# Kernel optimization log

Measured on AMD Instinct MI355X. Metric: run time of the kernel, lower is better.

## Reference

```python
import jax, jax.numpy as jnp
import numpy as np

EPS = 1e-5


def _shift1d(x, s, axis):
    """out[..., y, ...] = linear interp of x at position y + s along `axis`,
    zero-padded outside (== grid_sample bilinear, padding_mode='zeros',
    align_corners=True, for a pure axis-aligned shift of s pixels)."""
    n = x.shape[axis]
    f = jnp.floor(s)
    frac = (s - f).astype(x.dtype)  # scalar in [0,1)
    fi = f.astype(jnp.int32)

    def gather(off):
        idx = jnp.arange(n) + fi + off
        mask = (idx >= 0) & (idx < n)
        v = jnp.take(x, jnp.clip(idx, 0, n - 1), axis=axis)
        mshape = [1] * x.ndim
        mshape[axis] = n
        return v * mask.reshape(mshape).astype(x.dtype)

    return (1 - frac) * gather(0) + frac * gather(1)


def _axial_dw(x, w_h, w_w, r):
    """ContinuousAxialDW: x + depthwise learnable-dilation conv along H and W.
    w_h, w_w: (C, k) per-channel taps."""
    r = jnp.maximum(r, 1.0)
    c = x.shape[1]
    kh = w_h.shape[1]
    kw = w_w.shape[1]
    acc_h = jnp.zeros_like(x)
    for i, off in enumerate(range(-(kh // 2), kh // 2 + 1)):
        acc_h = acc_h + _shift1d(x, off * r, 2) * w_h[:, i].reshape(1, c, 1, 1)
    acc_w = jnp.zeros_like(x)
    for i, off in enumerate(range(-(kw // 2), kw // 2 + 1)):
        acc_w = acc_w + _shift1d(x, off * r, 3) * w_w[:, i].reshape(1, c, 1, 1)
    return x + acc_h + acc_w


def _bn(x, g, b, m, v):
    sh = (1, -1, 1, 1)
    scale = g.reshape(sh) * jax.lax.rsqrt(v.reshape(sh) + EPS)
    return (x - m.reshape(sh)) * scale + b.reshape(sh)


def _prelu(x, a):
    return jnp.where(x >= 0, x, a.reshape(1, -1, 1, 1) * x)


def _pw(w, x):  # 1x1 conv, no bias. w: (O, C)
    return jnp.einsum('oc,bchw->bohw', w, x)


def _dwconv3(x, w, axis):  # depthwise 3-tap conv, 'same' zero padding. w: (C, 3)
    c = x.shape[1]
    n = x.shape[axis]
    pad = [(0, 0)] * 4
    pad[axis] = (1, 1)
    xp = jnp.pad(x, pad)
    out = jnp.zeros_like(x)
    for i in range(3):
        out = out + jax.lax.slice_in_dim(xp, i, i + n, axis=axis) * w[:, i].reshape(1, c, 1, 1)
    return out


def _coord_att(x, w1, bn1, a1, wh, ww):
    n, c, h, w = x.shape
    xh = x.mean(axis=3, keepdims=True)                     # (n,c,h,1)
    xw = jnp.transpose(x.mean(axis=2, keepdims=True), (0, 1, 3, 2))  # (n,c,w,1)
    y = jnp.concatenate([xh, xw], axis=2)                  # (n,c,h+w,1)
    y = _prelu(_bn(_pw(w1, y), *bn1), a1)                  # (n,mip,h+w,1)
    yh, yw = y[:, :, :h], jnp.transpose(y[:, :, h:], (0, 1, 3, 2))
    a_h = jax.nn.sigmoid(_pw(wh, yh))                      # (n,c,h,1)
    a_w = jax.nn.sigmoid(_pw(ww, yw))                      # (n,c,1,w)
    return x * a_w * a_h


def _forward(x, r_m, wh_m, ww_m, r_l, wh_l, ww_l, w_fuse,
             bnf_g, bnf_b, bnf_m, bnf_v,
             dg_wh, dg_ww, dg_g, dg_b, dg_m, dg_v, act_a,
             ca_w1, ca_g, ca_b, ca_m, ca_v, ca_a, ca_wh, ca_ww):
    m = _axial_dw(x, wh_m, ww_m, r_m)
    l = _axial_dw(x, wh_l, ww_l, r_l)
    fused = _bn(_pw(w_fuse, m + l), bnf_g, bnf_b, bnf_m, bnf_v)
    edges = _dwconv3(x, dg_wh, 2) + _dwconv3(x, dg_ww, 3)
    anchor = _bn(x + edges, dg_g, dg_b, dg_m, dg_v)
    out = _prelu(fused + anchor, act_a)
    return _coord_att(out, ca_w1, (ca_g, ca_b, ca_m, ca_v), ca_a, ca_wh, ca_ww)


def setup_inputs() -> dict:
    key = jax.random.key(0)
    ks = jax.random.split(key, 16)
    B, C, H, W = 8, 96, 128, 128
    K = 5      # mixer kernel taps
    MIP = 8    # max(8, C // 32)

    def rn(k, shape, scale=1.0):
        return jax.random.normal(k, shape, dtype=jnp.float32) * scale

    f32 = jnp.float32
    return {
        'x': rn(ks[0], (B, C, H, W)),
        'r_m': jnp.array(4.0, f32),
        'wh_m': rn(ks[1], (C, K), 0.2), 'ww_m': rn(ks[2], (C, K), 0.2),
        'r_l': jnp.array(8.0, f32),
        'wh_l': rn(ks[3], (C, K), 0.2), 'ww_l': rn(ks[4], (C, K), 0.2),
        'w_fuse': rn(ks[5], (C, C), 0.1),
        'bnf_g': jnp.ones((C,), f32), 'bnf_b': jnp.zeros((C,), f32),
        'bnf_m': jnp.zeros((C,), f32), 'bnf_v': jnp.ones((C,), f32),
        'dg_wh': rn(ks[6], (C, 3), 0.3), 'dg_ww': rn(ks[7], (C, 3), 0.3),
        'dg_g': jnp.ones((C,), f32), 'dg_b': jnp.zeros((C,), f32),
        'dg_m': jnp.zeros((C,), f32), 'dg_v': jnp.ones((C,), f32),
        'act_a': jnp.full((C,), 0.25, f32),
        'ca_w1': rn(ks[8], (MIP, C), 0.1),
        'ca_g': jnp.ones((MIP,), f32), 'ca_b': jnp.zeros((MIP,), f32),
        'ca_m': jnp.zeros((MIP,), f32), 'ca_v': jnp.ones((MIP,), f32),
        'ca_a': jnp.full((MIP,), 0.25, f32),
        'ca_wh': rn(ks[9], (C, MIP), 0.3),
        'ca_ww': rn(ks[10], (C, MIP), 0.3),
    }


def reference(x, r_m, wh_m, ww_m, r_l, wh_l, ww_l, w_fuse,
              bnf_g, bnf_b, bnf_m, bnf_v,
              dg_wh, dg_ww, dg_g, dg_b, dg_m, dg_v, act_a,
              ca_w1, ca_g, ca_b, ca_m, ca_v, ca_a, ca_wh, ca_ww):
    return _forward(x, r_m, wh_m, ww_m, r_l, wh_l, ww_l, w_fuse,
                    bnf_g, bnf_b, bnf_m, bnf_v,
                    dg_wh, dg_ww, dg_g, dg_b, dg_m, dg_v, act_a,
                    ca_w1, ca_g, ca_b, ca_m, ca_v, ca_a, ca_wh, ca_ww)
```

## Files before the change

kernel.cpp:

```cpp
#include <hip/hip_runtime.h>
#include <hip/hip_bf16.h>
#include <math.h>

#define Bn 8
#define Cn 96
#define Hn 128
#define Wn 128
#define PLANE (Hn*Wn)
#define NIMG (Bn*Cn*PLANE)
#define EPSV 1e-5f
#define TAPN 48
#define TAPF 8

typedef __attribute__((ext_vector_type(8))) short short8;
typedef __attribute__((ext_vector_type(4))) float floatx4;

union FragU { short8 v; uint2 u2[2]; };

__global__ void k0_taps(
    const float* __restrict__ rm_p, const float* __restrict__ whm, const float* __restrict__ wwm,
    const float* __restrict__ rl_p, const float* __restrict__ whl, const float* __restrict__ wwl,
    int* __restrict__ cnt, int* __restrict__ offs, float* __restrict__ wts)
{
    int t = threadIdx.x;
    if (t >= Cn * 2) return;
    int c = t >> 1, dir = t & 1;
    for (int k = 0; k < TAPN; ++k) { offs[t * TAPN + k] = 0; wts[t * TAPN + k] = 0.f; }
    const float* tap_m = dir ? (wwm + c * 5) : (whm + c * 5);
    const float* tap_l = dir ? (wwl + c * 5) : (whl + c * 5);
    float rm = fmaxf(rm_p[0], 1.f), rl = fmaxf(rl_p[0], 1.f);
    float dense[TAPN];
    for (int k = 0; k < TAPN; ++k) dense[k] = 0.f;
    for (int pass = 0; pass < 2; ++pass) {
        float r = pass ? rl : rm;
        const float* tp = pass ? tap_l : tap_m;
        for (int i = 0; i < 5; ++i) {
            float s = (float)(i - 2) * r;
            float f = floorf(s);
            float fr = s - f;
            int fi = (int)f + 23;
            if (fi >= 0 && fi < TAPN)         dense[fi]     += tp[i] * (1.f - fr);
            if (fi + 1 >= 0 && fi + 1 < TAPN) dense[fi + 1] += tp[i] * fr;
        }
    }
    int n = 0;
    for (int k = 0; k < TAPN; ++k) {
        if (dense[k] != 0.f) {
            offs[t * TAPN + n] = k - 23;
            wts[t * TAPN + n] = dense[k];
            ++n;
        }
    }
    cnt[t] = n;
}

__global__ __launch_bounds__(512) void k1_axial(
    const float* __restrict__ x,
    const int* __restrict__ cnt, const int* __restrict__ offs, const float* __restrict__ wts,
    const float* __restrict__ dwh, const float* __restrict__ dww,
    const float* __restrict__ dg, const float* __restrict__ db_,
    const float* __restrict__ dm, const float* __restrict__ dv,
    short* __restrict__ t_bf, float* __restrict__ anchor)
{
    __shared__ float pl[Hn][160];

    int bc  = blockIdx.x;
    int b   = bc / Cn;
    int c   = bc % Cn;
    int tid = threadIdx.x;

    const float* plane = x + ((long)bc << 14);

    const float4* p4 = (const float4*)plane;
#pragma unroll
    for (int it = 0; it < 8; ++it) {
        int idx = tid + it * 512;
        int r = idx >> 5, c4 = idx & 31;
        *(float4*)&pl[r][16 + c4 * 4] = p4[idx];
    }
#pragma unroll
    for (int it = 0; it < 2; ++it) {
        int idx = tid + it * 512;
        int r = idx >> 3, pq = idx & 7;
        int col = (pq < 4) ? pq * 4 : 144 + (pq - 4) * 4;
        *(float4*)&pl[r][col] = (float4){0.f, 0.f, 0.f, 0.f};
    }

    int cH = cnt[c * 2], cW = cnt[c * 2 + 1];
    int soH[TAPF], soW[TAPF];
    float swH[TAPF], swW[TAPF];
#pragma unroll
    for (int j = 0; j < TAPF; ++j) {
        soH[j] = offs[(c * 2) * TAPN + j];
        swH[j] = wts[(c * 2) * TAPN + j];
        soW[j] = offs[(c * 2 + 1) * TAPN + j];
        swW[j] = wts[(c * 2 + 1) * TAPN + j];
    }
    bool fast = (cH <= TAPF) && (cW <= TAPF);
#pragma unroll
    for (int j = 0; j < TAPF; ++j)
        fast = fast && (soW[j] >= -16) && (soW[j] <= 16);

    float e0 = dwh[c * 3], e1 = dwh[c * 3 + 1], e2 = dwh[c * 3 + 2];
    float f0 = dww[c * 3], f1 = dww[c * 3 + 1], f2 = dww[c * 3 + 2];
    float dsc = dg[c] * rsqrtf(dv[c] + EPSV);
    float dof = db_[c] - dm[c] * dsc;

    __syncthreads();

    int m      = tid & 31;
    int rowgrp = tid >> 5;
    short* tbase = t_bf + ((long)(b * Hn) * Cn + c) * Wn;
    float* abase = anchor + ((long)bc << 14);

    for (int k = 0; k < 8; ++k) {
        int h = k * 16 + rowgrp;
        float vc0 = pl[h][16 + m];
        float vc1 = pl[h][16 + m + 32];
        float vc2 = pl[h][16 + m + 64];
        float vc3 = pl[h][16 + m + 96];
        float a0 = 2.f * vc0, a1 = 2.f * vc1, a2 = 2.f * vc2, a3 = 2.f * vc3;

        if (fast) {
#pragma unroll
            for (int j = 0; j < TAPF; ++j) {
                int y = h + soH[j];
                float wt = (y >= 0 && y < Hn) ? swH[j] : 0.f;
                y = min(max(y, 0), Hn - 1);
                a0 += wt * pl[y][16 + m];
                a1 += wt * pl[y][16 + m + 32];
                a2 += wt * pl[y][16 + m + 64];
                a3 += wt * pl[y][16 + m + 96];
            }
#pragma unroll
            for (int j = 0; j < TAPF; ++j) {
                int o = soW[j];
                float wt = swW[j];
                a0 += wt * pl[h][16 + m + o];
                a1 += wt * pl[h][16 + m + 32 + o];
                a2 += wt * pl[h][16 + m + 64 + o];
                a3 += wt * pl[h][16 + m + 96 + o];
            }
        } else {
            const int*   goH = offs + (c * 2 + 0) * TAPN;
            const float* gwH = wts  + (c * 2 + 0) * TAPN;
            const int*   goW = offs + (c * 2 + 1) * TAPN;
            const float* gwW = wts  + (c * 2 + 1) * TAPN;
            for (int j = 0; j < cH; ++j) {
                int y = h + goH[j];
                if (y >= 0 && y < Hn) {
                    float wt = gwH[j];
                    const float* rp = plane + (y << 7);
                    a0 += wt * rp[m];
                    a1 += wt * rp[m + 32];
                    a2 += wt * rp[m + 64];
                    a3 += wt * rp[m + 96];
                }
            }
            for (int j = 0; j < cW; ++j) {
                int o = goW[j];
                float wt = gwW[j];
                const float* rp = plane + (h << 7);
#pragma unroll
                for (int q = 0; q < 4; ++q) {
                    int xw = m + 32 * q + o;
                    float v = (xw >= 0 && xw < Wn) ? rp[xw] : 0.f;
                    float* ap = (q == 0) ? &a0 : (q == 1) ? &a1 : (q == 2) ? &a2 : &a3;
                    *ap += wt * v;
                }
            }
        }

        short* tp = tbase + (long)h * (Cn * Wn);
        {
            __hip_bfloat16 h0 = __float2bfloat16(a0), h1 = __float2bfloat16(a1);
            __hip_bfloat16 h2 = __float2bfloat16(a2), h3 = __float2bfloat16(a3);
            tp[m]      = *(short*)&h0;
            tp[m + 32] = *(short*)&h1;
            tp[m + 64] = *(short*)&h2;
            tp[m + 96] = *(short*)&h3;
        }

        int yu = (h > 0) ? h - 1 : 0;
        int yd = (h < Hn - 1) ? h + 1 : Hn - 1;
        float wu = (h > 0) ? e0 : 0.f;
        float wd = (h < Hn - 1) ? e2 : 0.f;
        float* ap = abase + (h << 7);
#pragma unroll
        for (int q = 0; q < 4; ++q) {
            int col = 16 + m + 32 * q;
            float vcq = (q == 0) ? vc0 : (q == 1) ? vc1 : (q == 2) ? vc2 : vc3;
            float vu = pl[yu][col];
            float vd = pl[yd][col];
            float vl = pl[h][col - 1];
            float vr = pl[h][col + 1];
            float edges = wu * vu + e1 * vcq + wd * vd + f0 * vl + f1 * vcq + f2 * vr;
            ap[m + 32 * q] = (vcq + edges) * dsc + dof;
        }
    }
}

__global__ __launch_bounds__(256) void k2_pw(
    const short* __restrict__ t_bf, const float* __restrict__ anchor,
    const float* __restrict__ w_fuse,
    const float* __restrict__ bg, const float* __restrict__ bb,
    const float* __restrict__ bm, const float* __restrict__ bv,
    const float* __restrict__ act_a,
    float* __restrict__ out)
{
    __shared__ short wl[Cn * 100];
    __shared__ short tl[64 * 100];
    __shared__ float sfsc[Cn], sfof[Cn], saa[Cn];

    int tid  = threadIdx.x;
    int blk  = blockIdx.x;
    int b    = blk >> 8;
    int r    = blk & 255;
    int h    = r >> 1;
    int hb   = r & 1;
    int lane = tid & 63;
    int wv   = tid >> 6;
    int n16  = lane & 15;
    int quad = lane >> 4;

    {
        uint* wdst = (uint*)wl;
        for (int e = tid; e < Cn * 48; e += 256) {
            int o = e / 48, cq = e - o * 48;
            float f0 = w_fuse[o * Cn + 2 * cq];
            float f1 = w_fuse[o * Cn + 2 * cq + 1];
            __hip_bfloat16 h0 = __float2bfloat16(f0);
            __hip_bfloat16 h1 = __float2bfloat16(f1);
            uint u = (uint)(*(unsigned short*)&h0) |
                     ((uint)(*(unsigned short*)&h1) << 16);
            wdst[o * 50 + cq] = u;
        }
    }
    if (tid < Cn) {
        float s = bg[tid] * rsqrtf(bv[tid] + EPSV);
        sfsc[tid] = s;
        sfof[tid] = bb[tid] - bm[tid] * s;
        saa[tid]  = act_a[tid];
    }
    {
        const uint* trow = (const uint*)t_bf + (size_t)(b * Hn + h) * Cn * 64 + hb * 32;
#pragma unroll
        for (int rep = 0; rep < 3; ++rep) {
            int task = tid + rep * 256;
            int cg = task >> 5, j = task & 31;
            int c0 = cg * 4;
            uint v0 = trow[(c0 + 0) * 64 + j];
            uint v1 = trow[(c0 + 1) * 64 + j];
            uint v2 = trow[(c0 + 2) * 64 + j];
            uint v3 = trow[(c0 + 3) * 64 + j];
            uint2 lo, hi;
            lo.x = (v0 & 0xffffu) | (v1 << 16);
            lo.y = (v2 & 0xffffu) | (v3 << 16);
            hi.x = (v0 >> 16) | (v1 & 0xffff0000u);
            hi.y = (v2 >> 16) | (v3 & 0xffff0000u);
            *(uint2*)(tl + (2 * j) * 100 + c0)     = lo;
            *(uint2*)(tl + (2 * j + 1) * 100 + c0) = hi;
        }
    }
    __syncthreads();

    FragU Bf[3];
    {
        int p = wv * 16 + n16;
        const short* bp = tl + p * 100 + quad * 8;
#pragma unroll
        for (int kb = 0; kb < 3; ++kb) {
            Bf[kb].u2[0] = *(const uint2*)(bp + kb * 32);
            Bf[kb].u2[1] = *(const uint2*)(bp + kb * 32 + 4);
        }
    }

    floatx4 acc[6];
#pragma unroll
    for (int mt = 0; mt < 6; ++mt)
        acc[mt] = (floatx4){0.f, 0.f, 0.f, 0.f};

#pragma unroll
    for (int mt = 0; mt < 6; ++mt) {
        int o = mt * 16 + n16;
        const short* apg = wl + o * 100 + quad * 8;
        FragU Af[3];
#pragma unroll
        for (int kb = 0; kb < 3; ++kb) {
            Af[kb].u2[0] = *(const uint2*)(apg + kb * 32);
            Af[kb].u2[1] = *(const uint2*)(apg + kb * 32 + 4);
        }
#pragma unroll
        for (int kb = 0; kb < 3; ++kb)
            acc[mt] = __builtin_amdgcn_mfma_f32_16x16x32_bf16(
                Af[kb].v, Bf[kb].v, acc[mt], 0, 0, 0);
    }

    long base = (long)b * Cn * PLANE + (h << 7) + hb * 64;
    int p = wv * 16 + n16;
#pragma unroll
    for (int mt = 0; mt < 6; ++mt) {
#pragma unroll
        for (int reg = 0; reg < 4; ++reg) {
            int o = mt * 16 + quad * 4 + reg;
            long idx = base + (long)o * PLANE + p;
            float fused = acc[mt][reg] * sfsc[o] + sfof[o];
            float v = fused + anchor[idx];
            out[idx] = (v >= 0.f) ? v : saa[o] * v;
        }
    }
}

__global__ __launch_bounds__(256) void k3_means(
    const float* __restrict__ op, float* __restrict__ xh, float* __restrict__ xw)
{
    int bc = blockIdx.x;
    const float4* pl = (const float4*)(op + ((long)bc << 14));
    int tid = threadIdx.x;
    int wq = tid & 31;
    int hg = tid >> 5;
    __shared__ float cpart[8][Wn + 4];
    __shared__ float rpart[Hn];
    float4 csum = make_float4(0, 0, 0, 0);
#pragma unroll
    for (int k = 0; k < 16; ++k) {
        int h = hg * 16 + k;
        float4 v = pl[h * 32 + wq];
        csum.x += v.x; csum.y += v.y; csum.z += v.z; csum.w += v.w;
        float rs = v.x + v.y + v.z + v.w;
#pragma unroll
        for (int off = 16; off; off >>= 1) rs += __shfl_down(rs, off, 32);
        if (wq == 0) rpart[h] = rs * (1.f / Wn);
    }
    cpart[hg][wq * 4 + 0] = csum.x;
    cpart[hg][wq * 4 + 1] = csum.y;
    cpart[hg][wq * 4 + 2] = csum.z;
    cpart[hg][wq * 4 + 3] = csum.w;
    __syncthreads();
    if (tid < 128) {
        float s = 0.f;
#pragma unroll
        for (int g = 0; g < 8; ++g) s += cpart[g][tid];
        xw[bc * Wn + tid] = s * (1.f / Hn);
        xh[bc * Hn + tid] = rpart[tid];
    }
}

__global__ __launch_bounds__(256) void k4a_y2(
    const float* __restrict__ xh, const float* __restrict__ xw,
    const float* __restrict__ w1,
    const float* __restrict__ g, const float* __restrict__ bb,
    const float* __restrict__ m, const float* __restrict__ v,
    const float* __restrict__ aa,
    float* __restrict__ y2)
{
    __shared__ float w1s[8 * Cn];
    __shared__ float part[4][16][8];

    int blk = blockIdx.x;
    int b   = blk >> 4;
    int pg  = blk & 15;
    int tid = threadIdx.x;
    for (int e = tid; e < 8 * Cn; e += 256) w1s[e] = w1[e];
    __syncthreads();

    int pl  = tid & 15;
    int cgl = (tid >> 4) & 3;
    int wv  = tid >> 6;
    int P   = pg * 16 + pl;
    int cg  = wv * 4 + cgl;

    const float* src = (P < Hn) ? (xh + (long)(b * Cn) * Hn + P)
                                : (xw + (long)(b * Cn) * Wn + (P - Hn));
    float acc[8];
#pragma unroll
    for (int i = 0; i < 8; ++i) acc[i] = 0.f;
#pragma unroll
    for (int ci = 0; ci < 6; ++ci) {
        int c = cg * 6 + ci;
        float yv = src[(long)c * Hn];
#pragma unroll
        for (int mip = 0; mip < 8; ++mip) acc[mip] += w1s[mip * Cn + c] * yv;
    }
#pragma unroll
    for (int mip = 0; mip < 8; ++mip) {
        acc[mip] += __shfl_xor(acc[mip], 16);
        acc[mip] += __shfl_xor(acc[mip], 32);
    }
    if (cgl == 0) {
#pragma unroll
        for (int mip = 0; mip < 8; ++mip) part[wv][pl][mip] = acc[mip];
    }
    __syncthreads();

    if (tid < 128) {
        int mip = tid >> 4, pl2 = tid & 15;
        float s = part[0][pl2][mip] + part[1][pl2][mip]
                + part[2][pl2][mip] + part[3][pl2][mip];
        float sc = g[mip] * rsqrtf(v[mip] + EPSV);
        float t = (s - m[mip]) * sc + bb[mip];
        float yv = (t >= 0.f) ? t : aa[mip] * t;
        y2[((long)b * 8 + mip) * 256 + pg * 16 + pl2] = yv;
    }
}

__global__ __launch_bounds__(256) void k4b_att(
    const float* __restrict__ y2,
    const float* __restrict__ cwh, const float* __restrict__ cww,
    float* __restrict__ a_h, float* __restrict__ a_w)
{
    int bc  = blockIdx.x;
    int b   = bc / Cn;
    int c   = bc % Cn;
    int tid = threadIdx.x;
    int p   = tid & 127;
    int isw = tid >> 7;

    const float* wsel = isw ? (cww + c * 8) : (cwh + c * 8);
    const float* ysrc = y2 + (long)b * 8 * 256 + (isw ? 128 : 0) + p;
    float s = 0.f;
#pragma unroll
    for (int mip = 0; mip < 8; ++mip) s += wsel[mip] * ysrc[mip * 256];
    float av = 1.f / (1.f + expf(-s));
    (isw ? a_w : a_h)[bc * Hn + p] = av;
}

__global__ __launch_bounds__(256) void k5_final(
    const float* __restrict__ a_h, const float* __restrict__ a_w,
    float* __restrict__ out)
{
    int idx = blockIdx.x * 256 + threadIdx.x;
    int e = idx * 4;
    if (e >= NIMG) return;
    int w = e & 127;
    int h = (e >> 7) & 127;
    int bc = e >> 14;
    float4 vv = *(const float4*)(out + e);
    float ah = a_h[bc * Hn + h];
    float4 aw = *(const float4*)(a_w + bc * Wn + w);
    float4 r;
    r.x = vv.x * ah * aw.x;
    r.y = vv.y * ah * aw.y;
    r.z = vv.z * ah * aw.z;
    r.w = vv.w * ah * aw.w;
    *(float4*)(out + e) = r;
}

extern "C" void kernel_launch(void* const* d_in, const int* in_sizes, int n_in,
                              void* d_out, int out_size, void* d_ws, size_t ws_size,
                              hipStream_t stream)
{
    const float* x     = (const float*)d_in[0];
    const float* r_m   = (const float*)d_in[1];
    const float* wh_m  = (const float*)d_in[2];
    const float* ww_m  = (const float*)d_in[3];
    const float* r_l   = (const float*)d_in[4];
    const float* wh_l  = (const float*)d_in[5];
    const float* ww_l  = (const float*)d_in[6];
    const float* wfuse = (const float*)d_in[7];
    const float* bnf_g = (const float*)d_in[8];
    const float* bnf_b = (const float*)d_in[9];
    const float* bnf_m = (const float*)d_in[10];
    const float* bnf_v = (const float*)d_in[11];
    const float* dg_wh = (const float*)d_in[12];
    const float* dg_ww = (const float*)d_in[13];
    const float* dg_g  = (const float*)d_in[14];
    const float* dg_b  = (const float*)d_in[15];
    const float* dg_m  = (const float*)d_in[16];
    const float* dg_v  = (const float*)d_in[17];
    const float* act_a = (const float*)d_in[18];
    const float* ca_w1 = (const float*)d_in[19];
    const float* ca_g  = (const float*)d_in[20];
    const float* ca_b  = (const float*)d_in[21];
    const float* ca_m  = (const float*)d_in[22];
    const float* ca_v  = (const float*)d_in[23];
    const float* ca_a  = (const float*)d_in[24];
    const float* ca_wh = (const float*)d_in[25];
    const float* ca_ww = (const float*)d_in[26];

    float* ws     = (float*)d_ws;
    float* anchor = ws;
    float* xh     = anchor + (size_t)NIMG;
    float* xw     = xh + Bn * Cn * Hn;
    float* a_h    = xw + Bn * Cn * Wn;
    float* a_w    = a_h + Bn * Cn * Hn;
    float* y2     = a_w + Bn * Cn * Wn;
    float* wts    = y2 + Bn * 8 * 256;
    int*   cnt    = (int*)(wts + 2 * Cn * TAPN);
    int*   offs   = cnt + 2 * Cn;
    short* t_bf   = (short*)(offs + 2 * Cn * TAPN);

    float* out = (float*)d_out;

    hipLaunchKernelGGL(k0_taps, dim3(1), dim3(256), 0, stream,
                       r_m, wh_m, ww_m, r_l, wh_l, ww_l, cnt, offs, wts);
    hipLaunchKernelGGL(k1_axial, dim3(Bn * Cn), dim3(512), 0, stream,
                       x, cnt, offs, wts, dg_wh, dg_ww, dg_g, dg_b, dg_m, dg_v,
                       t_bf, anchor);
    hipLaunchKernelGGL(k2_pw, dim3(Bn * Hn * 2), dim3(256), 0, stream,
                       t_bf, anchor, wfuse, bnf_g, bnf_b, bnf_m, bnf_v, act_a, out);
    hipLaunchKernelGGL(k3_means, dim3(Bn * Cn), dim3(256), 0, stream,
                       out, xh, xw);
    hipLaunchKernelGGL(k4a_y2, dim3(Bn * 16), dim3(256), 0, stream,
                       xh, xw, ca_w1, ca_g, ca_b, ca_m, ca_v, ca_a, y2);
    hipLaunchKernelGGL(k4b_att, dim3(Bn * Cn), dim3(256), 0, stream,
                       y2, ca_wh, ca_ww, a_h, a_w);
    hipLaunchKernelGGL(k5_final, dim3(NIMG / 1024), dim3(256), 0, stream,
                       a_h, a_w, out);
}
```

Measured before the change: 257.2 us.

## Fuse coord-attention kernels into one attention-and-scale pass; split means reduction

Three small kernels (y2 projection, attention sigmoid, final scaling) become one kernel per (b,c) plane. It recomputes the 96-channel projection for its own channel, builds the attention vectors in shared memory and rescales the output plane in place. The means kernel now splits each plane into four row blocks and accumulates column sums with atomicAdd into a buffer that k1 zeroes. This removes two launches and the global round trips for y2, a_h and a_w. The cost is redundant projection work in every block (each of the 768 blocks recomputes the 96-channel y2 for its batch) and float atomics, which make column sums order-nondeterministic.

```diff
diff --git a/kernel.cpp b/kernel.cpp
--- a/kernel.cpp
+++ b/kernel.cpp
@@ -60,7 +60,8 @@
     const float* __restrict__ dwh, const float* __restrict__ dww,
     const float* __restrict__ dg, const float* __restrict__ db_,
     const float* __restrict__ dm, const float* __restrict__ dv,
-    short* __restrict__ t_bf, float* __restrict__ anchor)
+    short* __restrict__ t_bf, float* __restrict__ anchor,
+    float* __restrict__ xw_zero)
 {
     __shared__ float pl[Hn][160];
 
@@ -68,6 +69,8 @@
     int b   = bc / Cn;
     int c   = bc % Cn;
     int tid = threadIdx.x;
+
+    if (tid < Wn) xw_zero[bc * Wn + tid] = 0.f;
 
     const float* plane = x + ((long)bc << 14);
 
@@ -314,23 +317,25 @@
 __global__ __launch_bounds__(256) void k3_means(
     const float* __restrict__ op, float* __restrict__ xh, float* __restrict__ xw)
 {
-    int bc = blockIdx.x;
-    const float4* pl = (const float4*)(op + ((long)bc << 14));
+    int blk = blockIdx.x;
+    int bc  = blk >> 2;
+    int q   = blk & 3;
+    const float4* pl = (const float4*)(op + ((long)bc << 14) + (q << 12));
     int tid = threadIdx.x;
     int wq = tid & 31;
     int hg = tid >> 5;
     __shared__ float cpart[8][Wn + 4];
-    __shared__ float rpart[Hn];
+    __shared__ float rpart[32];
     float4 csum = make_float4(0, 0, 0, 0);
 #pragma unroll
-    for (int k = 0; k < 16; ++k) {
-        int h = hg * 16 + k;
-        float4 v = pl[h * 32 + wq];
+    for (int k = 0; k < 4; ++k) {
+        int hl = hg * 4 + k;
+        float4 v = pl[hl * 32 + wq];
         csum.x += v.x; csum.y += v.y; csum.z += v.z; csum.w += v.w;
         float rs = v.x + v.y + v.z + v.w;
 #pragma unroll
         for (int off = 16; off; off >>= 1) rs += __shfl_down(rs, off, 32);
-        if (wq == 0) rpart[h] = rs * (1.f / Wn);
+        if (wq == 0) rpart[hl] = rs * (1.f / Wn);
     }
     cpart[hg][wq * 4 + 0] = csum.x;
     cpart[hg][wq * 4 + 1] = csum.y;
@@ -341,109 +346,74 @@
         float s = 0.f;
 #pragma unroll
         for (int g = 0; g < 8; ++g) s += cpart[g][tid];
-        xw[bc * Wn + tid] = s * (1.f / Hn);
-        xh[bc * Hn + tid] = rpart[tid];
-    }
-}
-
-__global__ __launch_bounds__(256) void k4a_y2(
+        atomicAdd(&xw[bc * Wn + tid], s);
+    }
+    if (tid < 32) xh[bc * Hn + q * 32 + tid] = rpart[tid];
+}
+
+__global__ __launch_bounds__(256) void kf_att_scale(
     const float* __restrict__ xh, const float* __restrict__ xw,
     const float* __restrict__ w1,
     const float* __restrict__ g, const float* __restrict__ bb,
     const float* __restrict__ m, const float* __restrict__ v,
     const float* __restrict__ aa,
-    float* __restrict__ y2)
+    const float* __restrict__ cwh, const float* __restrict__ cww,
+    float* __restrict__ out)
 {
     __shared__ float w1s[8 * Cn];
-    __shared__ float part[4][16][8];
-
-    int blk = blockIdx.x;
-    int b   = blk >> 4;
-    int pg  = blk & 15;
-    int tid = threadIdx.x;
-    for (int e = tid; e < 8 * Cn; e += 256) w1s[e] = w1[e];
-    __syncthreads();
-
-    int pl  = tid & 15;
-    int cgl = (tid >> 4) & 3;
-    int wv  = tid >> 6;
-    int P   = pg * 16 + pl;
-    int cg  = wv * 4 + cgl;
-
-    const float* src = (P < Hn) ? (xh + (long)(b * Cn) * Hn + P)
-                                : (xw + (long)(b * Cn) * Wn + (P - Hn));
-    float acc[8];
-#pragma unroll
-    for (int i = 0; i < 8; ++i) acc[i] = 0.f;
-#pragma unroll
-    for (int ci = 0; ci < 6; ++ci) {
-        int c = cg * 6 + ci;
-        float yv = src[(long)c * Hn];
-#pragma unroll
-        for (int mip = 0; mip < 8; ++mip) acc[mip] += w1s[mip * Cn + c] * yv;
-    }
-#pragma unroll
-    for (int mip = 0; mip < 8; ++mip) {
-        acc[mip] += __shfl_xor(acc[mip], 16);
-        acc[mip] += __shfl_xor(acc[mip], 32);
-    }
-    if (cgl == 0) {
-#pragma unroll
-        for (int mip = 0; mip < 8; ++mip) part[wv][pl][mip] = acc[mip];
-    }
-    __syncthreads();
-
-    if (tid < 128) {
-        int mip = tid >> 4, pl2 = tid & 15;
-        float s = part[0][pl2][mip] + part[1][pl2][mip]
-                + part[2][pl2][mip] + part[3][pl2][mip];
-        float sc = g[mip] * rsqrtf(v[mip] + EPSV);
-        float t = (s - m[mip]) * sc + bb[mip];
-        float yv = (t >= 0.f) ? t : aa[mip] * t;
-        y2[((long)b * 8 + mip) * 256 + pg * 16 + pl2] = yv;
-    }
-}
-
-__global__ __launch_bounds__(256) void k4b_att(
-    const float* __restrict__ y2,
-    const float* __restrict__ cwh, const float* __restrict__ cww,
-    float* __restrict__ a_h, float* __restrict__ a_w)
-{
+    __shared__ float sah[Hn];
+    __shared__ float saw[Wn];
+
     int bc  = blockIdx.x;
     int b   = bc / Cn;
     int c   = bc % Cn;
-    int tid = threadIdx.x;
-    int p   = tid & 127;
-    int isw = tid >> 7;
-
-    const float* wsel = isw ? (cww + c * 8) : (cwh + c * 8);
-    const float* ysrc = y2 + (long)b * 8 * 256 + (isw ? 128 : 0) + p;
+    int p   = threadIdx.x;
+
+    for (int e = p; e < 8 * Cn; e += 256) w1s[e] = w1[e];
+    __syncthreads();
+
+    bool isH = (p < Hn);
+    const float* src = isH ? (xh + ((long)b * Cn) * Hn + p)
+                           : (xw + ((long)b * Cn) * Wn + (p - Hn));
+    float scale = isH ? 1.f : (1.f / Hn);
+
+    float acc[8];
+#pragma unroll
+    for (int i = 0; i < 8; ++i) acc[i] = 0.f;
+    for (int cc = 0; cc < Cn; ++cc) {
+        float yv = src[(long)cc * Hn] * scale;
+#pragma unroll
+        for (int mip = 0; mip < 8; ++mip) acc[mip] += w1s[mip * Cn + cc] * yv;
+    }
+    const float* wsel = isH ? (cwh + c * 8) : (cww + c * 8);
     float s = 0.f;
 #pragma unroll
-    for (int mip = 0; mip < 8; ++mip) s += wsel[mip] * ysrc[mip * 256];
+    for (int mip = 0; mip < 8; ++mip) {
+        float sc = g[mip] * rsqrtf(v[mip] + EPSV);
+        float t = (acc[mip] - m[mip]) * sc + bb[mip];
+        float yv = (t >= 0.f) ? t : aa[mip] * t;
+        s += wsel[mip] * yv;
+    }
     float av = 1.f / (1.f + expf(-s));
-    (isw ? a_w : a_h)[bc * Hn + p] = av;
-}
-
-__global__ __launch_bounds__(256) void k5_final(
-    const float* __restrict__ a_h, const float* __restrict__ a_w,
-    float* __restrict__ out)
-{
-    int idx = blockIdx.x * 256 + threadIdx.x;
-    int e = idx * 4;
-    if (e >= NIMG) return;
-    int w = e & 127;
-    int h = (e >> 7) & 127;
-    int bc = e >> 14;
-    float4 vv = *(const float4*)(out + e);
-    float ah = a_h[bc * Hn + h];
-    float4 aw = *(const float4*)(a_w + bc * Wn + w);
-    float4 r;
-    r.x = vv.x * ah * aw.x;
-    r.y = vv.y * ah * aw.y;
-    r.z = vv.z * ah * aw.z;
-    r.w = vv.w * ah * aw.w;
-    *(float4*)(out + e) = r;
+    if (isH) sah[p] = av; else saw[p - Hn] = av;
+    __syncthreads();
+
+    float4* p4 = (float4*)(out + ((long)bc << 14));
+#pragma unroll
+    for (int it = 0; it < 16; ++it) {
+        int idx = p + it * 256;
+        int h = idx >> 5;
+        int w4 = idx & 31;
+        float4 vv = p4[idx];
+        float ah = sah[h];
+        float4 aw = *(float4*)&saw[w4 * 4];
+        float4 r;
+        r.x = vv.x * ah * aw.x;
+        r.y = vv.y * ah * aw.y;
+        r.z = vv.z * ah * aw.z;
+        r.w = vv.w * ah * aw.w;
+        p4[idx] = r;
+    }
 }
 
 extern "C" void kernel_launch(void* const* d_in, const int* in_sizes, int n_in,
@@ -482,10 +452,7 @@
     float* anchor = ws;
     float* xh     = anchor + (size_t)NIMG;
     float* xw     = xh + Bn * Cn * Hn;
-    float* a_h    = xw + Bn * Cn * Wn;
-    float* a_w    = a_h + Bn * Cn * Hn;
-    float* y2     = a_w + Bn * Cn * Wn;
-    float* wts    = y2 + Bn * 8 * 256;
+    float* wts    = xw + Bn * Cn * Wn;
     int*   cnt    = (int*)(wts + 2 * Cn * TAPN);
     int*   offs   = cnt + 2 * Cn;
     short* t_bf   = (short*)(offs + 2 * Cn * TAPN);
@@ -496,15 +463,12 @@
                        r_m, wh_m, ww_m, r_l, wh_l, ww_l, cnt, offs, wts);
     hipLaunchKernelGGL(k1_axial, dim3(Bn * Cn), dim3(512), 0, stream,
                        x, cnt, offs, wts, dg_wh, dg_ww, dg_g, dg_b, dg_m, dg_v,
-                       t_bf, anchor);
+                       t_bf, anchor, xw);
     hipLaunchKernelGGL(k2_pw, dim3(Bn * Hn * 2), dim3(256), 0, stream,
                        t_bf, anchor, wfuse, bnf_g, bnf_b, bnf_m, bnf_v, act_a, out);
-    hipLaunchKernelGGL(k3_means, dim3(Bn * Cn), dim3(256), 0, stream,
+    hipLaunchKernelGGL(k3_means, dim3(Bn * Cn * 4), dim3(256), 0, stream,
                        out, xh, xw);
-    hipLaunchKernelGGL(k4a_y2, dim3(Bn * 16), dim3(256), 0, stream,
-                       xh, xw, ca_w1, ca_g, ca_b, ca_m, ca_v, ca_a, y2);
-    hipLaunchKernelGGL(k4b_att, dim3(Bn * Cn), dim3(256), 0, stream,
-                       y2, ca_wh, ca_ww, a_h, a_w);
-    hipLaunchKernelGGL(k5_final, dim3(NIMG / 1024), dim3(256), 0, stream,
-                       a_h, a_w, out);
-}
+    hipLaunchKernelGGL(kf_att_scale, dim3(Bn * Cn), dim3(256), 0, stream,
+                       xh, xw, ca_w1, ca_g, ca_b, ca_m, ca_v, ca_a, ca_wh, ca_ww,
+                       out);
+}
```

Result: no change. 255.4 us (-0.7%).
